# Kernel optimization log

Hardware: AMD Instinct MI355X
Metric: run time of the kernel (lower is better)

The kernel has to match this reference:

```python
import jax, jax.numpy as jnp
import numpy as np

N = 100000
E = 3200000
F_IN = 512
H = 128
C = 40


def gcn_conv(x, edge_index, edge_weight, W, b):
    """PyG GCNConv: x' = D^-1/2 (A+I) D^-1/2 (x W) + b, symmetric norm with self-loops."""
    n = x.shape[0]
    x = x @ W  # [N, H]
    row, col = edge_index[0], edge_index[1]
    sl = jnp.arange(n)
    row_f = jnp.concatenate([row, sl])
    col_f = jnp.concatenate([col, sl])
    w_f = jnp.concatenate([edge_weight, jnp.ones((n,), x.dtype)])
    deg = jax.ops.segment_sum(w_f, col_f, num_segments=n)  # in-degree incl. self-loop
    dinv = jnp.where(deg > 0, jax.lax.rsqrt(deg), 0.0)
    norm = dinv[row_f] * w_f * dinv[col_f]  # [E+N]
    msg = x[row_f] * norm[:, None]          # gather + scale
    out = jax.ops.segment_sum(msg, col_f, num_segments=n)  # scatter-add to targets
    return out + b


def setup_inputs() -> dict:
    key = jax.random.key(0)
    ks = jax.random.split(key, 12)
    inp = {
        "x": jax.random.normal(ks[0], (N, F_IN), jnp.float32),
        "edge_index": jax.random.randint(ks[1], (2, E), 0, N, jnp.int64),
        "edge_weight": jax.random.uniform(ks[2], (E,), jnp.float32),
        # first_lin
        "W1": jax.random.normal(ks[3], (F_IN, H), jnp.float32) / np.sqrt(F_IN),
        "b1": jnp.zeros((H,), jnp.float32),
        # conv layers (num_layers=2)
        "Wc1": jax.random.normal(ks[4], (H, H), jnp.float32) / np.sqrt(H),
        "bc1": jnp.zeros((H,), jnp.float32),
        "Wc2": jax.random.normal(ks[5], (H, H), jnp.float32) / np.sqrt(H),
        "bc2": jnp.zeros((H,), jnp.float32),
        # lin2
        "W2": jax.random.normal(ks[6], (H, C), jnp.float32) / np.sqrt(H),
        "b2": jnp.zeros((C,), jnp.float32),
        # wide layer
        "Ww": jax.random.normal(ks[7], (F_IN, C), jnp.float32) / np.sqrt(F_IN),
        "bw": jnp.zeros((C,), jnp.float32),
        # attention layer (-> 2 logits per node)
        "Wa": jax.random.normal(ks[8], (F_IN, 2), jnp.float32) / np.sqrt(F_IN),
        "ba": jnp.zeros((2,), jnp.float32),
    }
    return inp


def reference(x, edge_index, edge_weight, W1, b1, Wc1, bc1, Wc2, bc2, W2, b2, Ww, bw, Wa, ba):
    # deep branch (res_type=0.0, eval mode: dropout = identity)
    h = jax.nn.relu(x @ W1 + b1)
    h = jax.nn.relu(gcn_conv(h, edge_index, edge_weight, Wc1, bc1))
    h = jax.nn.relu(gcn_conv(h, edge_index, edge_weight, Wc2, bc2))
    deep_x = h @ W2 + b2  # [N, C]
    # wide branch on raw features
    wide_x = x @ Ww + bw  # [N, C]
    # attention fusion: softmax over 2 branch logits per node
    attn = jax.nn.softmax(x @ Wa + ba, axis=-1)  # [N, 2]
    out = deep_x * attn[:, 0:1] + wide_x * attn[:, 1:2]
    return out
```

## Files before the change

kernel.cpp:

```cpp
#include <hip/hip_runtime.h>
#include <hip/hip_bf16.h>
#include <cstdint>

#define N_NODES 100000
#define N_EDGES 3200000

typedef __attribute__((ext_vector_type(8))) short short8;
typedef __attribute__((ext_vector_type(4))) float floatx4;

#define FXS 8388608.0f
#define MASK40 0xFFFFFFFFFFull

__device__ __forceinline__ unsigned short f2bf(float f) {
    unsigned u = __float_as_uint(f);
    u += 0x7fff + ((u >> 16) & 1);
    return (unsigned short)(u >> 16);
}
__device__ __forceinline__ float bf2f(unsigned short s) {
    return __uint_as_float(((unsigned)s) << 16);
}
__device__ __forceinline__ float bflo(unsigned u) {
    return __uint_as_float(u << 16);
}
__device__ __forceinline__ float bfhi(unsigned u) {
    return __uint_as_float(u & 0xffff0000u);
}
__device__ __forceinline__ unsigned pack_bf2(float a, float b) {
    union { __hip_bfloat162 h2; unsigned u; } cv;
    cv.h2 = __float22bfloat162_rn(make_float2(a, b));
    return cv.u;
}

__global__ void setup_misc(const float* __restrict__ W1, const float* __restrict__ b1,
                           const float* __restrict__ Ww, const float* __restrict__ bw,
                           const float* __restrict__ Wa, const float* __restrict__ ba,
                           const float* __restrict__ Wc1, const float* __restrict__ Wc2,
                           unsigned short* __restrict__ WcatT, float* __restrict__ bcat,
                           unsigned short* __restrict__ Wc1T, unsigned short* __restrict__ Wc2T,
                           unsigned long long* __restrict__ packed, int n) {
    int bid = blockIdx.x, tid = threadIdx.x;
    if (bid < 192) {
        int c = bid;
        for (int kk = tid; kk < 512; kk += 256) {
            float v;
            if (c < 128)      v = W1[kk * 128 + c];
            else if (c < 168) v = Ww[kk * 40 + (c - 128)];
            else if (c < 170) v = Wa[kk * 2 + (c - 168)];
            else              v = 0.f;
            WcatT[(size_t)c * 512 + kk] = f2bf(v);
        }
        if (tid == 0) {
            float b;
            if (c < 128)      b = b1[c];
            else if (c < 168) b = bw[c - 128];
            else if (c < 170) b = ba[c - 168];
            else              b = 0.f;
            bcat[c] = b;
        }
    } else if (bid < 320) {
        int c = bid - 192;
        if (tid < 128) Wc1T[(size_t)c * 128 + tid] = f2bf(Wc1[tid * 128 + c]);
        else { int k = tid - 128; Wc2T[(size_t)c * 128 + k] = f2bf(Wc2[k * 128 + c]); }
    } else {
        int i = (bid - 320) * 256 + tid;
        if (i < n) packed[i] = 0ull;
    }
}

template <int EPI, int NT, int AF32>
__device__ __forceinline__ void gemm_body(
    int mblk, const void* __restrict__ Avoid, const unsigned short* __restrict__ BT,
    int M, int K,
    unsigned short* __restrict__ C0, float* __restrict__ C1, float* __restrict__ C2,
    const float* __restrict__ bias, const float* __restrict__ rowscale) {
    constexpr int NB = 32 * NT;
    __shared__ __align__(16) unsigned short Ast[64 * 40];
    __shared__ __align__(16) unsigned short Bst[NB * 40];

    int tid = threadIdx.x;
    int m0 = mblk * 64;
    int wave = tid >> 6, lane = tid & 63;
    int quad = lane >> 4, mi = lane & 15;
    int wm = (wave >> 1) * 32;
    int wn = (wave & 1) * (16 * NT);

    int srow = tid >> 2;
    int sk8 = (tid & 3) * 8;

    int arow = m0 + srow; if (arow >= M) arow = M - 1;

    floatx4 acc[2][NT] = {};

    for (int kc = 0; kc < K; kc += 32) {
        if (AF32) {
            const float* Af = (const float*)Avoid;
            const float4* ap = (const float4*)(Af + (size_t)arow * K + kc + sk8);
            float4 f0 = ap[0], f1 = ap[1];
            uint4 pk;
            pk.x = pack_bf2(f0.x, f0.y);
            pk.y = pack_bf2(f0.z, f0.w);
            pk.z = pack_bf2(f1.x, f1.y);
            pk.w = pack_bf2(f1.z, f1.w);
            *(uint4*)&Ast[srow * 40 + sk8] = pk;
        } else {
            const unsigned short* Ab = (const unsigned short*)Avoid;
            uint4 av = *(const uint4*)(Ab + (size_t)arow * K + kc + sk8);
            *(uint4*)&Ast[srow * 40 + sk8] = av;
        }
#pragma unroll
        for (int i = tid; i < NB * 4; i += 256) {
            int brow = i >> 2;
            int bk8 = (i & 3) * 8;
            uint4 bv = *(const uint4*)(BT + (size_t)brow * K + kc + bk8);
            *(uint4*)&Bst[brow * 40 + bk8] = bv;
        }
        __syncthreads();

        short8 a0 = *(const short8*)&Ast[(wm + mi) * 40 + quad * 8];
        short8 a1 = *(const short8*)&Ast[(wm + 16 + mi) * 40 + quad * 8];
#pragma unroll
        for (int nt = 0; nt < NT; ++nt) {
            short8 b = *(const short8*)&Bst[(wn + nt * 16 + mi) * 40 + quad * 8];
            acc[0][nt] = __builtin_amdgcn_mfma_f32_16x16x32_bf16(a0, b, acc[0][nt], 0, 0, 0);
            acc[1][nt] = __builtin_amdgcn_mfma_f32_16x16x32_bf16(a1, b, acc[1][nt], 0, 0, 0);
        }
        __syncthreads();
    }

#pragma unroll
    for (int mt = 0; mt < 2; ++mt) {
#pragma unroll
        for (int nt = 0; nt < NT; ++nt) {
            floatx4 v = acc[mt][nt];
            int gn = wn + nt * 16 + mi;
#pragma unroll
            for (int r = 0; r < 4; ++r) {
                int gm = m0 + wm + mt * 16 + quad * 4 + r;
                if (gm >= M) continue;
                float val = v[r];
                if (EPI == 0) {
                    C0[(size_t)gm * 128 + gn] = f2bf(rowscale[gm] * val);
                } else {
                    val += bias[gn];
                    if (gn < 128)      C0[(size_t)gm * 128 + gn] = f2bf(fmaxf(val, 0.f));
                    else if (gn < 168) C1[(size_t)gm * 40 + (gn - 128)] = val;
                    else if (gn < 170) C2[(size_t)gm * 2 + (gn - 168)] = val;
                }
            }
        }
    }
}

__global__ __launch_bounds__(256) void mega1(
    const float* __restrict__ x, const unsigned short* __restrict__ WcatT,
    unsigned short* __restrict__ h0, float* __restrict__ wide, float* __restrict__ attnL,
    const float* __restrict__ bcat,
    const int* __restrict__ ei, const float* __restrict__ ew,
    unsigned long long* __restrict__ packed, int* __restrict__ rank, int M, int e) {
    int bid = blockIdx.x;
    int q = bid / 9;
    if (bid - q * 9 == 0) {
        gemm_body<1, 6, 1>(q, x, WcatT, M, 512, h0, wide, attnL, bcat, nullptr);
    } else {
        int i = (bid - q - 1) * 256 + threadIdx.x;
        if (i < e) {
            int d = ei[e + i];
            unsigned fx = (unsigned)(ew[i] * FXS);
            unsigned long long old =
                atomicAdd(&packed[d], (1ull << 40) | (unsigned long long)fx);
            rank[i] = (int)(old >> 40);
        }
    }
}

__global__ __launch_bounds__(256) void mega2(
    const unsigned short* __restrict__ h0, const unsigned short* __restrict__ Wc1T,
    unsigned short* __restrict__ tmpB, const float* __restrict__ dinv,
    const int* __restrict__ ei, const float* __restrict__ ew,
    const int* __restrict__ ptr, const int* __restrict__ rank,
    uint2* __restrict__ edges, int M, int e) {
    int bid = blockIdx.x;
    int q = bid / 9;
    if (bid - q * 9 == 0) {
        gemm_body<0, 4, 0>(q, h0, Wc1T, M, 128, tmpB, nullptr, nullptr, nullptr, dinv);
    } else {
        int i = (bid - q - 1) * 256 + threadIdx.x;
        if (i < e) {
            int r = ei[i];
            int d = ei[e + i];
            edges[ptr[d] + rank[i]] = make_uint2((unsigned)r, __float_as_uint(ew[i]));
        }
    }
}

__global__ __launch_bounds__(256) void gemm_conv(
    const unsigned short* __restrict__ A, const unsigned short* __restrict__ BT,
    unsigned short* __restrict__ C0, const float* __restrict__ rowscale, int M) {
    gemm_body<0, 4, 0>(blockIdx.x, A, BT, M, 128, C0, nullptr, nullptr, nullptr, rowscale);
}

__global__ void scan_blocks(const unsigned long long* __restrict__ packed,
                            int* __restrict__ ptr, int* __restrict__ bsum,
                            float* __restrict__ dinv, int n) {
    __shared__ int s[1024];
    int tid = threadIdx.x;
    int i = blockIdx.x * 1024 + tid;
    int v = 0;
    if (i < n) {
        unsigned long long pk = packed[i];
        v = (int)(pk >> 40);
        float deg = 1.0f + (float)(pk & MASK40) * (1.0f / FXS);
        dinv[i] = rsqrtf(deg);
    }
    s[tid] = v;
    __syncthreads();
    for (int off = 1; off < 1024; off <<= 1) {
        int t = (tid >= off) ? s[tid - off] : 0;
        __syncthreads();
        s[tid] += t;
        __syncthreads();
    }
    if (i < n) ptr[i] = s[tid] - v;
    if (tid == 1023) bsum[blockIdx.x] = s[1023];
}

__global__ void scan_bsums(int* bsum, int nb) {
    __shared__ int s[1024];
    int tid = threadIdx.x;
    int v = (tid < nb) ? bsum[tid] : 0;
    s[tid] = v;
    __syncthreads();
    for (int off = 1; off < 1024; off <<= 1) {
        int t = (tid >= off) ? s[tid - off] : 0;
        __syncthreads();
        s[tid] += t;
        __syncthreads();
    }
    if (tid < nb) bsum[tid] = s[tid] - v;
}

__global__ void scan_add(int* __restrict__ ptr, const int* __restrict__ bsum,
                         int n, int total) {
    int i = blockIdx.x * 1024 + threadIdx.x;
    if (i < n) ptr[i] += bsum[blockIdx.x];
    if (i == 0) ptr[n] = total;
}

__global__ __launch_bounds__(256) void propagate(
    const unsigned int* __restrict__ tmp2,
    unsigned int* __restrict__ out2,
    const float* __restrict__ bias, const float* __restrict__ dinv,
    const int* __restrict__ ptr, const uint2* __restrict__ edges, int n) {
    int wave = threadIdx.x >> 6, lane = threadIdx.x & 63;
    int d = blockIdx.x * 4 + wave;
    if (d >= n) return;

    unsigned u = tmp2[(size_t)d * 64 + lane];
    float acc0 = bflo(u);
    float acc1 = bfhi(u);

    int p = ptr[d], p1 = ptr[d + 1];
    for (; p + 8 <= p1; p += 8) {
        uint2 q[8];
#pragma unroll
        for (int j = 0; j < 8; ++j) q[j] = edges[p + j];
        unsigned rv[8];
#pragma unroll
        for (int j = 0; j < 8; ++j) rv[j] = tmp2[(size_t)q[j].x * 64 + lane];
#pragma unroll
        for (int j = 0; j < 8; ++j) {
            float w = __uint_as_float(q[j].y);
            acc0 += w * bflo(rv[j]); acc1 += w * bfhi(rv[j]);
        }
    }
    for (; p < p1; ++p) {
        uint2 q = edges[p];
        unsigned a = tmp2[(size_t)q.x * 64 + lane];
        float w = __uint_as_float(q.y);
        acc0 += w * bflo(a); acc1 += w * bfhi(a);
    }
    float di = dinv[d];
    float v0 = fmaxf(di * acc0 + bias[2 * lane], 0.f);
    float v1 = fmaxf(di * acc1 + bias[2 * lane + 1], 0.f);
    out2[(size_t)d * 64 + lane] = (unsigned)f2bf(v0) | ((unsigned)f2bf(v1) << 16);
}

__global__ void final_k(const unsigned short* __restrict__ h2, const float* __restrict__ wide,
                        const float* __restrict__ attnL, const float* __restrict__ W2,
                        const float* __restrict__ b2, float* __restrict__ out) {
    __shared__ __align__(16) float hs[8][132];
    __shared__ __align__(16) float w2t[40][132];
    int tid = threadIdx.x;
    int m0 = blockIdx.x * 8;

    for (int idx = tid; idx < 8 * 128; idx += 320) {
        hs[idx >> 7][idx & 127] = bf2f(h2[(size_t)m0 * 128 + idx]);
    }
    for (int idx = tid; idx < 40 * 128; idx += 320) {
        int c = idx >> 7, k = idx & 127;
        w2t[c][k] = W2[k * 40 + c];
    }
    __syncthreads();

    int c = tid % 40;
    int nl = tid / 40;
    float acc = 0.f;
#pragma unroll
    for (int k = 0; k < 128; k += 4) {
        float4 h4 = *(const float4*)&hs[nl][k];
        float4 w4 = *(const float4*)&w2t[c][k];
        acc += h4.x * w4.x + h4.y * w4.y + h4.z * w4.z + h4.w * w4.w;
    }
    int m = m0 + nl;
    float l0 = attnL[m * 2], l1 = attnL[m * 2 + 1];
    float mx = fmaxf(l0, l1);
    float e0 = __expf(l0 - mx), e1 = __expf(l1 - mx);
    float inv = 1.f / (e0 + e1);
    out[(size_t)m * 40 + c] = (acc + b2[c]) * (e0 * inv) + wide[(size_t)m * 40 + c] * (e1 * inv);
}

extern "C" void kernel_launch(void* const* d_in, const int* in_sizes, int n_in,
                              void* d_out, int out_size, void* d_ws, size_t ws_size,
                              hipStream_t stream) {
    (void)in_sizes; (void)n_in; (void)out_size; (void)ws_size;
    const float* x   = (const float*)d_in[0];
    const int*   ei  = (const int*)d_in[1];
    const float* ew  = (const float*)d_in[2];
    const float* W1  = (const float*)d_in[3];
    const float* b1  = (const float*)d_in[4];
    const float* Wc1 = (const float*)d_in[5];
    const float* bc1 = (const float*)d_in[6];
    const float* Wc2 = (const float*)d_in[7];
    const float* bc2 = (const float*)d_in[8];
    const float* W2  = (const float*)d_in[9];
    const float* b2  = (const float*)d_in[10];
    const float* Ww  = (const float*)d_in[11];
    const float* bw  = (const float*)d_in[12];
    const float* Wa  = (const float*)d_in[13];
    const float* ba  = (const float*)d_in[14];
    float* out = (float*)d_out;

    const int N = N_NODES, E = N_EDGES;
    char* ws = (char*)d_ws;
    size_t off = 0;
    auto alloc = [&](size_t bytes) -> void* {
        void* p = ws + off;
        off = (off + bytes + 255) & ~(size_t)255;
        return p;
    };
    unsigned short* bufA = (unsigned short*)alloc((size_t)N * 128 * 2);
    unsigned short* bufB = (unsigned short*)alloc((size_t)N * 128 * 2);
    float* wide  = (float*)alloc((size_t)N * 40 * 4);
    float* attnL = (float*)alloc((size_t)N * 2 * 4);
    float* dinv  = (float*)alloc((size_t)N * 4);
    unsigned long long* packed = (unsigned long long*)alloc((size_t)N * 8);
    int*   ptr   = (int*)alloc((size_t)(N + 1) * 4);
    int*   rank  = (int*)alloc((size_t)E * 4);
    int*   bsum  = (int*)alloc(1024 * 4);
    uint2* edges = (uint2*)alloc((size_t)E * 8);
    unsigned short* WcatT = (unsigned short*)alloc((size_t)192 * 512 * 2);
    unsigned short* Wc1T  = (unsigned short*)alloc((size_t)128 * 128 * 2);
    unsigned short* Wc2T  = (unsigned short*)alloc((size_t)128 * 128 * 2);
    float* bcat  = (float*)alloc(192 * 4);

    const int MB = (N + 63) / 64;
    const int EB = (E + 255) / 256;
    const int MEGA = MB * 9;

    setup_misc<<<320 + (N + 255) / 256, 256, 0, stream>>>(
        W1, b1, Ww, bw, Wa, ba, Wc1, Wc2, WcatT, bcat, Wc1T, Wc2T, packed, N);

    mega1<<<MEGA, 256, 0, stream>>>(x, WcatT, bufA, wide, attnL, bcat,
                                    ei, ew, packed, rank, N, E);

    int nb = (N + 1023) / 1024;
    scan_blocks<<<nb, 1024, 0, stream>>>(packed, ptr, bsum, dinv, N);
    scan_bsums<<<1, 1024, 0, stream>>>(bsum, nb);
    scan_add<<<nb, 1024, 0, stream>>>(ptr, bsum, N, E);

    mega2<<<MEGA, 256, 0, stream>>>(bufA, Wc1T, bufB, dinv, ei, ew, ptr, rank, edges, N, E);
    propagate<<<(N + 3) / 4, 256, 0, stream>>>((const unsigned int*)bufB, (unsigned int*)bufA,
                                               bc1, dinv, ptr, edges, N);

    gemm_conv<<<MB, 256, 0, stream>>>(bufA, Wc2T, bufB, dinv, N);
    propagate<<<(N + 3) / 4, 256, 0, stream>>>((const unsigned int*)bufB, (unsigned int*)bufA,
                                               bc2, dinv, ptr, edges, N);

    final_k<<<N / 8, 320, 0, stream>>>(bufA, wide, attnL, W2, b2, out);
}
```

Baseline: 913.5 us.

## Replace global-atomic CSR build with two-pass bucketed radix sort via LDS atomics

Replaces the per-edge 64-bit global atomicAdd on a packed count/weight word with a two-level bucketed counting sort. Edges are first histogrammed and scattered into 391 destination buckets using shared-memory atomics, and the bucket-local pass then computes degrees, weighted sums and final CSR placement, also with LDS atomics. The goal is to remove contended global atomics and random scattered writes to the rank and edges arrays. In exchange it adds more kernel launches, an extra intermediate edge buffer and a second scan, and it packs the low destination bits into the source index, which assumes source ids fit in 24 bits.

```diff
diff --git a/kernel.cpp b/kernel.cpp
--- a/kernel.cpp
+++ b/kernel.cpp
@@ -9,7 +9,9 @@
 typedef __attribute__((ext_vector_type(4))) float floatx4;
 
 #define FXS 8388608.0f
-#define MASK40 0xFFFFFFFFFFull
+#define EA 320
+#define EPB 10000
+#define NBKT 391
 
 __device__ __forceinline__ unsigned short f2bf(float f) {
     unsigned u = __float_as_uint(f);
@@ -36,8 +38,7 @@
                            const float* __restrict__ Wa, const float* __restrict__ ba,
                            const float* __restrict__ Wc1, const float* __restrict__ Wc2,
                            unsigned short* __restrict__ WcatT, float* __restrict__ bcat,
-                           unsigned short* __restrict__ Wc1T, unsigned short* __restrict__ Wc2T,
-                           unsigned long long* __restrict__ packed, int n) {
+                           unsigned short* __restrict__ Wc1T, unsigned short* __restrict__ Wc2T) {
     int bid = blockIdx.x, tid = threadIdx.x;
     if (bid < 192) {
         int c = bid;
@@ -57,13 +58,10 @@
             else              b = 0.f;
             bcat[c] = b;
         }
-    } else if (bid < 320) {
+    } else {
         int c = bid - 192;
         if (tid < 128) Wc1T[(size_t)c * 128 + tid] = f2bf(Wc1[tid * 128 + c]);
         else { int k = tid - 128; Wc2T[(size_t)c * 128 + k] = f2bf(Wc2[k * 128 + c]); }
-    } else {
-        int i = (bid - 320) * 256 + tid;
-        if (i < n) packed[i] = 0ull;
     }
 }
 
@@ -151,45 +149,100 @@
     }
 }
 
-__global__ __launch_bounds__(256) void mega1(
+__global__ __launch_bounds__(256) void megaA(
     const float* __restrict__ x, const unsigned short* __restrict__ WcatT,
     unsigned short* __restrict__ h0, float* __restrict__ wide, float* __restrict__ attnL,
-    const float* __restrict__ bcat,
+    const float* __restrict__ bcat, const int* __restrict__ ei,
+    int* __restrict__ histA, int M, int e) {
+    int bid = blockIdx.x;
+    if (bid >= EA) {
+        gemm_body<1, 6, 1>(bid - EA, x, WcatT, M, 512, h0, wide, attnL, bcat, nullptr);
+        return;
+    }
+    __shared__ unsigned lh[NBKT];
+    int tid = threadIdx.x;
+    for (int i = tid; i < NBKT; i += 256) lh[i] = 0;
+    __syncthreads();
+    int base = bid * EPB, end = base + EPB; if (end > e) end = e;
+    for (int i = base + tid; i < end; i += 256) {
+        int d = ei[e + i];
+        atomicAdd(&lh[d >> 8], 1u);
+    }
+    __syncthreads();
+    for (int k = tid; k < NBKT; k += 256) histA[k * EA + bid] = (int)lh[k];
+}
+
+__global__ __launch_bounds__(256) void scatterA(
     const int* __restrict__ ei, const float* __restrict__ ew,
-    unsigned long long* __restrict__ packed, int* __restrict__ rank, int M, int e) {
-    int bid = blockIdx.x;
-    int q = bid / 9;
-    if (bid - q * 9 == 0) {
-        gemm_body<1, 6, 1>(q, x, WcatT, M, 512, h0, wide, attnL, bcat, nullptr);
-    } else {
-        int i = (bid - q - 1) * 256 + threadIdx.x;
-        if (i < e) {
-            int d = ei[e + i];
-            unsigned fx = (unsigned)(ew[i] * FXS);
-            unsigned long long old =
-                atomicAdd(&packed[d], (1ull << 40) | (unsigned long long)fx);
-            rank[i] = (int)(old >> 40);
-        }
-    }
-}
-
-__global__ __launch_bounds__(256) void mega2(
+    const int* __restrict__ offA, uint2* __restrict__ cs, int e) {
+    int bid = blockIdx.x, tid = threadIdx.x;
+    __shared__ unsigned lh[NBKT];
+    __shared__ int lo[NBKT];
+    for (int i = tid; i < NBKT; i += 256) { lh[i] = 0; lo[i] = offA[i * EA + bid]; }
+    __syncthreads();
+    int base = bid * EPB, end = base + EPB; if (end > e) end = e;
+    for (int i = base + tid; i < end; i += 256) {
+        int d = ei[e + i];
+        int r = ei[i];
+        float w = ew[i];
+        int k = d >> 8;
+        unsigned lr = atomicAdd(&lh[k], 1u);
+        cs[lo[k] + (int)lr] = make_uint2((unsigned)r | ((unsigned)(d & 255) << 24),
+                                         __float_as_uint(w));
+    }
+}
+
+__global__ __launch_bounds__(1024) void passB1(
+    const uint2* __restrict__ cs, const int* __restrict__ offA,
+    int* __restrict__ cnt, unsigned* __restrict__ wsum, int n, int e) {
+    int k = blockIdx.x, tid = threadIdx.x;
+    __shared__ unsigned lc[256], lw[256];
+    if (tid < 256) { lc[tid] = 0; lw[tid] = 0; }
+    __syncthreads();
+    int start = offA[k * EA];
+    int end = (k == NBKT - 1) ? e : offA[(k + 1) * EA];
+    for (int i = start + tid; i < end; i += 1024) {
+        uint2 u = cs[i];
+        int dlow = u.x >> 24;
+        unsigned fx = (unsigned)(__uint_as_float(u.y) * FXS);
+        atomicAdd(&lc[dlow], 1u);
+        atomicAdd(&lw[dlow], fx);
+    }
+    __syncthreads();
+    if (tid < 256) {
+        int d = (k << 8) + tid;
+        if (d < n) { cnt[d] = (int)lc[tid]; wsum[d] = lw[tid]; }
+    }
+}
+
+__global__ void dinv_k(const unsigned* __restrict__ wsum, float* __restrict__ dinv, int n) {
+    int i = blockIdx.x * 256 + threadIdx.x;
+    if (i < n) dinv[i] = rsqrtf(1.0f + (float)wsum[i] * (1.0f / FXS));
+}
+
+__global__ __launch_bounds__(256) void megaB(
     const unsigned short* __restrict__ h0, const unsigned short* __restrict__ Wc1T,
     unsigned short* __restrict__ tmpB, const float* __restrict__ dinv,
-    const int* __restrict__ ei, const float* __restrict__ ew,
-    const int* __restrict__ ptr, const int* __restrict__ rank,
-    uint2* __restrict__ edges, int M, int e) {
+    const uint2* __restrict__ cs, const int* __restrict__ offA,
+    const int* __restrict__ ptr, uint2* __restrict__ edges, int M, int n, int e) {
     int bid = blockIdx.x;
-    int q = bid / 9;
-    if (bid - q * 9 == 0) {
-        gemm_body<0, 4, 0>(q, h0, Wc1T, M, 128, tmpB, nullptr, nullptr, nullptr, dinv);
-    } else {
-        int i = (bid - q - 1) * 256 + threadIdx.x;
-        if (i < e) {
-            int r = ei[i];
-            int d = ei[e + i];
-            edges[ptr[d] + rank[i]] = make_uint2((unsigned)r, __float_as_uint(ew[i]));
-        }
+    if (bid >= NBKT) {
+        gemm_body<0, 4, 0>(bid - NBKT, h0, Wc1T, M, 128, tmpB, nullptr, nullptr, nullptr, dinv);
+        return;
+    }
+    int k = bid, tid = threadIdx.x;
+    __shared__ unsigned lc[256];
+    __shared__ int lp[256];
+    { lc[tid] = 0; int d = (k << 8) + tid; lp[tid] = (d < n) ? ptr[d] : 0; }
+    __syncthreads();
+    int start = offA[k * EA];
+    int end = (k == NBKT - 1) ? e : offA[(k + 1) * EA];
+    for (int i = start + tid; i < end; i += 256) {
+        uint2 u = cs[i];
+        int dlow = u.x >> 24;
+        unsigned src = u.x & 0x00FFFFFFu;
+        unsigned lr = atomicAdd(&lc[dlow], 1u);
+        edges[lp[dlow] + (int)lr] = make_uint2(src, u.y);
     }
 }
 
@@ -199,19 +252,12 @@
     gemm_body<0, 4, 0>(blockIdx.x, A, BT, M, 128, C0, nullptr, nullptr, nullptr, rowscale);
 }
 
-__global__ void scan_blocks(const unsigned long long* __restrict__ packed,
-                            int* __restrict__ ptr, int* __restrict__ bsum,
-                            float* __restrict__ dinv, int n) {
+__global__ void scan1(const int* __restrict__ in, int* __restrict__ out,
+                      int* __restrict__ bsum, int n) {
     __shared__ int s[1024];
     int tid = threadIdx.x;
     int i = blockIdx.x * 1024 + tid;
-    int v = 0;
-    if (i < n) {
-        unsigned long long pk = packed[i];
-        v = (int)(pk >> 40);
-        float deg = 1.0f + (float)(pk & MASK40) * (1.0f / FXS);
-        dinv[i] = rsqrtf(deg);
-    }
+    int v = (i < n) ? in[i] : 0;
     s[tid] = v;
     __syncthreads();
     for (int off = 1; off < 1024; off <<= 1) {
@@ -220,7 +266,7 @@
         s[tid] += t;
         __syncthreads();
     }
-    if (i < n) ptr[i] = s[tid] - v;
+    if (i < n) out[i] = s[tid] - v;
     if (tid == 1023) bsum[blockIdx.x] = s[1023];
 }
 
@@ -239,11 +285,11 @@
     if (tid < nb) bsum[tid] = s[tid] - v;
 }
 
-__global__ void scan_add(int* __restrict__ ptr, const int* __restrict__ bsum,
-                         int n, int total) {
+__global__ void scan_add(int* __restrict__ out, const int* __restrict__ bsum,
+                         int n, int tailv) {
     int i = blockIdx.x * 1024 + threadIdx.x;
-    if (i < n) ptr[i] += bsum[blockIdx.x];
-    if (i == 0) ptr[n] = total;
+    if (i < n) out[i] += bsum[blockIdx.x];
+    if (i == 0 && tailv >= 0) out[n] = tailv;
 }
 
 __global__ __launch_bounds__(256) void propagate(
@@ -353,9 +399,11 @@
     float* wide  = (float*)alloc((size_t)N * 40 * 4);
     float* attnL = (float*)alloc((size_t)N * 2 * 4);
     float* dinv  = (float*)alloc((size_t)N * 4);
-    unsigned long long* packed = (unsigned long long*)alloc((size_t)N * 8);
+    int*   histA = (int*)alloc((size_t)NBKT * EA * 4);
+    uint2* cs    = (uint2*)alloc((size_t)E * 8);
+    int*   cnt   = (int*)alloc((size_t)N * 4);
+    unsigned* wsum = (unsigned*)alloc((size_t)N * 4);
     int*   ptr   = (int*)alloc((size_t)(N + 1) * 4);
-    int*   rank  = (int*)alloc((size_t)E * 4);
     int*   bsum  = (int*)alloc(1024 * 4);
     uint2* edges = (uint2*)alloc((size_t)E * 8);
     unsigned short* WcatT = (unsigned short*)alloc((size_t)192 * 512 * 2);
@@ -364,21 +412,31 @@
     float* bcat  = (float*)alloc(192 * 4);
 
     const int MB = (N + 63) / 64;
-    const int EB = (E + 255) / 256;
-    const int MEGA = MB * 9;
-
-    setup_misc<<<320 + (N + 255) / 256, 256, 0, stream>>>(
-        W1, b1, Ww, bw, Wa, ba, Wc1, Wc2, WcatT, bcat, Wc1T, Wc2T, packed, N);
-
-    mega1<<<MEGA, 256, 0, stream>>>(x, WcatT, bufA, wide, attnL, bcat,
-                                    ei, ew, packed, rank, N, E);
-
-    int nb = (N + 1023) / 1024;
-    scan_blocks<<<nb, 1024, 0, stream>>>(packed, ptr, bsum, dinv, N);
-    scan_bsums<<<1, 1024, 0, stream>>>(bsum, nb);
-    scan_add<<<nb, 1024, 0, stream>>>(ptr, bsum, N, E);
-
-    mega2<<<MEGA, 256, 0, stream>>>(bufA, Wc1T, bufB, dinv, ei, ew, ptr, rank, edges, N, E);
+    const int NHA = NBKT * EA;
+
+    setup_misc<<<320, 256, 0, stream>>>(W1, b1, Ww, bw, Wa, ba, Wc1, Wc2,
+                                        WcatT, bcat, Wc1T, Wc2T);
+
+    megaA<<<EA + MB, 256, 0, stream>>>(x, WcatT, bufA, wide, attnL, bcat,
+                                       ei, histA, N, E);
+
+    int nbA = (NHA + 1023) / 1024;
+    scan1<<<nbA, 1024, 0, stream>>>(histA, histA, bsum, NHA);
+    scan_bsums<<<1, 1024, 0, stream>>>(bsum, nbA);
+    scan_add<<<nbA, 1024, 0, stream>>>(histA, bsum, NHA, -1);
+
+    scatterA<<<EA, 256, 0, stream>>>(ei, ew, histA, cs, E);
+
+    passB1<<<NBKT, 1024, 0, stream>>>(cs, histA, cnt, wsum, N, E);
+    dinv_k<<<(N + 255) / 256, 256, 0, stream>>>(wsum, dinv, N);
+
+    int nbC = (N + 1023) / 1024;
+    scan1<<<nbC, 1024, 0, stream>>>(cnt, ptr, bsum, N);
+    scan_bsums<<<1, 1024, 0, stream>>>(bsum, nbC);
+    scan_add<<<nbC, 1024, 0, stream>>>(ptr, bsum, N, E);
+
+    megaB<<<NBKT + MB, 256, 0, stream>>>(bufA, Wc1T, bufB, dinv,
+                                         cs, histA, ptr, edges, N, N, E);
     propagate<<<(N + 3) / 4, 256, 0, stream>>>((const unsigned int*)bufB, (unsigned int*)bufA,
                                                bc1, dinv, ptr, edges, N);
 
```

New measurement: 854.9 us. -6.4%, faster.
